# Optimization experiments

Hardware: AMD Instinct MI355X
Metric: run time of the kernel (lower is better)

Reference implementation:

```python
import jax, jax.numpy as jnp
import numpy as np

DROPOUT_RATE = 0.1  # reference runs deterministically (dropout disabled), matching eval-mode math


def setup_inputs() -> dict:
    key = jax.random.key(0)
    k1, k2, k3 = jax.random.split(key, 3)
    BH, S, D = 32, 2048, 64   # batch*heads, seq_len, d_head
    B = 2                      # true batch (mask batch dim)
    q = jax.random.normal(k1, (BH, S, D), dtype=jnp.float32)
    k = jax.random.normal(k2, (BH, S, D), dtype=jnp.float32)
    v = jax.random.normal(k3, (BH, S, D), dtype=jnp.float32)
    mask = jnp.zeros((B, S, S), dtype=jnp.float32)  # additive mask
    return {"q": q, "k": k, "v": v, "mask": mask}


def reference(q, k, v, mask):
    # Scaled dot-product attention with additive mask.
    # q,k,v: [BH, S, D]; mask: [B, S, S], tiled along batch to BH.
    dk = jnp.asarray(k.shape[-1], dtype=jnp.float32)
    scores = jnp.einsum('bqd,bkd->bqk', q, k) / jnp.sqrt(dk)  # [BH, S, S]
    reps = q.shape[0] // mask.shape[0]
    mask_t = jnp.tile(mask, (reps, 1, 1))                     # [BH, S, S]
    attn = jax.nn.softmax(scores + mask_t, axis=-1)
    out = jnp.einsum('bqk,bkd->bqd', attn, v)                 # [BH, S, D]
    # K.dropout omitted: deterministic reference (eval mode / identity)
    return out
```

## Files before the change

### kernel.cpp

```cpp
#include <hip/hip_runtime.h>


constexpr int cBH = 32;
constexpr int cS  = 2048;
constexpr int cD  = 64;
constexpr int cQT = 128;
constexpr int cNT = cS / 64;

typedef __bf16 bf16x8 __attribute__((ext_vector_type(8)));
typedef __bf16 bf16x4 __attribute__((ext_vector_type(4)));
typedef float  f32x4  __attribute__((ext_vector_type(4)));

__device__ __forceinline__ unsigned short bfbits(float f) {
    return __builtin_bit_cast(unsigned short, (__bf16)f);
}
__device__ __forceinline__ bf16x4 pack4(f32x4 a) {
    bf16x4 r;
    r[0] = (__bf16)a[0]; r[1] = (__bf16)a[1];
    r[2] = (__bf16)a[2]; r[3] = (__bf16)a[3];
    return r;
}
__device__ __forceinline__ bf16x8 pack8(f32x4 a, f32x4 b) {
    bf16x8 r;
    r[0] = (__bf16)a[0]; r[1] = (__bf16)a[1];
    r[2] = (__bf16)a[2]; r[3] = (__bf16)a[3];
    r[4] = (__bf16)b[0]; r[5] = (__bf16)b[1];
    r[6] = (__bf16)b[2]; r[7] = (__bf16)b[3];
    return r;
}
__device__ __forceinline__ int fkey(int row) {
    return ((row & 7) ^ ((row >> 3) << 1)) & 7;
}

__global__ __launch_bounds__(512, 4)
void sdpa_flash_kernel(const float* __restrict__ q,
                       const float* __restrict__ k,
                       const float* __restrict__ v,
                       const float* __restrict__ mask,
                       float* __restrict__ out)
{
    __shared__ unsigned short sK[2][64 * 64];
    __shared__ unsigned short sV[2][64 * 64];
    __shared__ unsigned short sP[8][16 * 64];

    const int tid  = threadIdx.x;
    const int wv   = tid >> 6;
    const int lane = tid & 63;
    const int quad = lane >> 4;
    const int ln   = lane & 15;

    const int fid = blockIdx.x;
    const int bh  = (fid & 7) | ((fid >> 7) << 3);
    const int qb  = ((fid >> 3) & 15) * cQT;
    const int mb  = bh & 1;

    bf16x8 aq0, aq1;
    {
        const float* qp = q + ((size_t)bh * cS + qb + wv * 16 + ln) * cD + quad * 8;
        aq0 = pack8(*(const f32x4*)(qp),      *(const f32x4*)(qp + 4));
        aq1 = pack8(*(const f32x4*)(qp + 32), *(const f32x4*)(qp + 36));
    }

    f32x4 acc[4];
    float lsum[4];
#pragma unroll
    for (int t = 0; t < 4; ++t) acc[t] = (f32x4){0.f, 0.f, 0.f, 0.f};
#pragma unroll
    for (int r = 0; r < 4; ++r) lsum[r] = 0.f;

    const float L2E = 1.4426950408889634f;
    const float SCL = 0.125f * L2E;

    const int srow = tid >> 4;
    const int col4 = (tid & 15) << 2;
    const int ka0  = srow * 64 + (((col4 >> 3) ^ (srow & 7)) << 3) + (col4 & 7);
    const int ka1  = ka0 + 32 * 64;
    const float* kg = k + (size_t)bh * cS * cD;
    const float* vg = v + (size_t)bh * cS * cD;
    const int g0 = tid * 4, g1 = 2048 + tid * 4;
    const float* mbase = mask + (size_t)mb * cS * cS
                              + (size_t)(qb + wv * 16 + quad * 4) * cS + ln;

    f32x4 K0 = *(const f32x4*)(kg + g0);
    f32x4 K1 = *(const f32x4*)(kg + g1);
    f32x4 V0 = *(const f32x4*)(vg + g0);
    f32x4 V1 = *(const f32x4*)(vg + g1);
    *(bf16x4*)&sK[0][ka0] = pack4(K0);
    *(bf16x4*)&sK[0][ka1] = pack4(K1);
#pragma unroll
    for (int j = 0; j < 4; ++j) {
        int d = col4 + j, g = (d ^ (d >> 3)) & 7;
        sV[0][d * 64 + (((srow >> 3) ^ g) << 3) + (srow & 7)]       = bfbits(V0[j]);
        sV[0][d * 64 + ((((srow >> 3) + 4) ^ g) << 3) + (srow & 7)] = bfbits(V1[j]);
    }

    for (int kt = 0; kt < cNT; ++kt) {
        const int cur = kt & 1;
        const unsigned short* sKc = sK[cur];
        const unsigned short* sVc = sV[cur];

        if (kt + 1 < cNT) {
            const int tb = (kt + 1) * 4096;
            K0 = *(const f32x4*)(kg + tb + g0);
            K1 = *(const f32x4*)(kg + tb + g1);
            V0 = *(const f32x4*)(vg + tb + g0);
            V1 = *(const f32x4*)(vg + tb + g1);
        }

        __syncthreads();

        float mrg[4][4];
#pragma unroll
        for (int nt = 0; nt < 4; ++nt)
#pragma unroll
            for (int r = 0; r < 4; ++r)
                mrg[nt][r] = mbase[(size_t)r * cS + kt * 64 + nt * 16];

        float p4[4][4];
#pragma unroll
        for (int nt = 0; nt < 4; ++nt) {
            f32x4 c = (f32x4){0.f, 0.f, 0.f, 0.f};
#pragma unroll
            for (int ks = 0; ks < 2; ++ks) {
                bf16x8 b = *(const bf16x8*)(
                    &sKc[(nt * 16 + ln) * 64 + ((((ks << 2) | quad) ^ (ln & 7)) << 3)]);
                c = __builtin_amdgcn_mfma_f32_16x16x32_bf16(ks ? aq1 : aq0, b, c, 0, 0, 0);
            }
#pragma unroll
            for (int r = 0; r < 4; ++r)
                p4[nt][r] = __builtin_amdgcn_exp2f(c[r] * SCL + mrg[nt][r] * L2E);
        }
#pragma unroll
        for (int r = 0; r < 4; ++r)
            lsum[r] += (p4[0][r] + p4[1][r]) + (p4[2][r] + p4[3][r]);

#pragma unroll
        for (int nt = 0; nt < 4; ++nt)
#pragma unroll
            for (int r = 0; r < 4; ++r) {
                int row = quad * 4 + r;
                int blk = ((nt * 2 + (ln >> 3)) ^ fkey(row)) << 3;
                sP[wv][row * 64 + blk + (ln & 7)] = bfbits(p4[nt][r]);
            }

#pragma unroll
        for (int ks = 0; ks < 2; ++ks) {
            bf16x8 ap = *(const bf16x8*)(
                &sP[wv][ln * 64 + ((((ks << 2) | quad) ^ fkey(ln)) << 3)]);
#pragma unroll
            for (int dt = 0; dt < 4; ++dt) {
                int d = dt * 16 + ln, g = (d ^ (d >> 3)) & 7;
                bf16x8 bv = *(const bf16x8*)(
                    &sVc[d * 64 + ((((ks << 2) | quad) ^ g) << 3)]);
                acc[dt] = __builtin_amdgcn_mfma_f32_16x16x32_bf16(ap, bv, acc[dt], 0, 0, 0);
            }
        }

        if (kt + 1 < cNT) {
            unsigned short* sKn = sK[cur ^ 1];
            unsigned short* sVn = sV[cur ^ 1];
            *(bf16x4*)&sKn[ka0] = pack4(K0);
            *(bf16x4*)&sKn[ka1] = pack4(K1);
#pragma unroll
            for (int j = 0; j < 4; ++j) {
                int d = col4 + j, g = (d ^ (d >> 3)) & 7;
                sVn[d * 64 + (((srow >> 3) ^ g) << 3) + (srow & 7)]       = bfbits(V0[j]);
                sVn[d * 64 + ((((srow >> 3) + 4) ^ g) << 3) + (srow & 7)] = bfbits(V1[j]);
            }
        }
    }

#pragma unroll
    for (int off = 1; off < 16; off <<= 1)
#pragma unroll
        for (int r = 0; r < 4; ++r)
            lsum[r] += __shfl_xor(lsum[r], off, 64);
    float rl[4];
#pragma unroll
    for (int r = 0; r < 4; ++r) rl[r] = 1.0f / lsum[r];
#pragma unroll
    for (int dt = 0; dt < 4; ++dt)
#pragma unroll
        for (int r = 0; r < 4; ++r)
            out[((size_t)bh * cS + qb + wv * 16 + quad * 4 + r) * cD + dt * 16 + ln]
                = acc[dt][r] * rl[r];
}

extern "C" void kernel_launch(void* const* d_in, const int* in_sizes, int n_in,
                              void* d_out, int out_size, void* d_ws, size_t ws_size,
                              hipStream_t stream) {
    const float* q = (const float*)d_in[0];
    const float* k = (const float*)d_in[1];
    const float* v = (const float*)d_in[2];
    const float* m = (const float*)d_in[3];
    float* o = (float*)d_out;
    sdpa_flash_kernel<<<dim3(512), 512, 0, stream>>>(q, k, v, m, o);
}
```

Before: 213.0 us.

## Software-pipeline PV matmul one tile behind QK, prefetch mask, prescale Q

The P·V product for tile kt-1 now runs after the QK/softmax of tile kt, using a triple-buffered V array and a double-buffered per-wave P buffer, so the two MFMA phases can interleave and the P store-to-load latency is hidden. Mask values for the next tile are prefetched into registers along with K/V instead of being loaded after the barrier. Q is prescaled by the softmax scale times log2(e) at load time, which removes a multiply per score. The cost is extra LDS (one more V buffer plus doubled P buffers) and more registers, which may hurt occupancy at the launch bound of four blocks per CU. The Q prescale also rounds slightly differently in bf16.

```diff
diff --git a/kernel.cpp b/kernel.cpp
--- a/kernel.cpp
+++ b/kernel.cpp
@@ -20,12 +20,12 @@
     r[2] = (__bf16)a[2]; r[3] = (__bf16)a[3];
     return r;
 }
-__device__ __forceinline__ bf16x8 pack8(f32x4 a, f32x4 b) {
+__device__ __forceinline__ bf16x8 pack8s(f32x4 a, f32x4 b, float s) {
     bf16x8 r;
-    r[0] = (__bf16)a[0]; r[1] = (__bf16)a[1];
-    r[2] = (__bf16)a[2]; r[3] = (__bf16)a[3];
-    r[4] = (__bf16)b[0]; r[5] = (__bf16)b[1];
-    r[6] = (__bf16)b[2]; r[7] = (__bf16)b[3];
+    r[0] = (__bf16)(a[0]*s); r[1] = (__bf16)(a[1]*s);
+    r[2] = (__bf16)(a[2]*s); r[3] = (__bf16)(a[3]*s);
+    r[4] = (__bf16)(b[0]*s); r[5] = (__bf16)(b[1]*s);
+    r[6] = (__bf16)(b[2]*s); r[7] = (__bf16)(b[3]*s);
     return r;
 }
 __device__ __forceinline__ int fkey(int row) {
@@ -40,8 +40,8 @@
                        float* __restrict__ out)
 {
     __shared__ unsigned short sK[2][64 * 64];
-    __shared__ unsigned short sV[2][64 * 64];
-    __shared__ unsigned short sP[8][16 * 64];
+    __shared__ unsigned short sV[3][64 * 64];
+    __shared__ unsigned short sP[8][2][16 * 64];
 
     const int tid  = threadIdx.x;
     const int wv   = tid >> 6;
@@ -54,11 +54,13 @@
     const int qb  = ((fid >> 3) & 15) * cQT;
     const int mb  = bh & 1;
 
+    const float L2E = 1.4426950408889634f;
+
     bf16x8 aq0, aq1;
     {
         const float* qp = q + ((size_t)bh * cS + qb + wv * 16 + ln) * cD + quad * 8;
-        aq0 = pack8(*(const f32x4*)(qp),      *(const f32x4*)(qp + 4));
-        aq1 = pack8(*(const f32x4*)(qp + 32), *(const f32x4*)(qp + 36));
+        aq0 = pack8s(*(const f32x4*)(qp),      *(const f32x4*)(qp + 4),  0.125f * L2E);
+        aq1 = pack8s(*(const f32x4*)(qp + 32), *(const f32x4*)(qp + 36), 0.125f * L2E);
     }
 
     f32x4 acc[4];
@@ -67,9 +69,6 @@
     for (int t = 0; t < 4; ++t) acc[t] = (f32x4){0.f, 0.f, 0.f, 0.f};
 #pragma unroll
     for (int r = 0; r < 4; ++r) lsum[r] = 0.f;
-
-    const float L2E = 1.4426950408889634f;
-    const float SCL = 0.125f * L2E;
 
     const int srow = tid >> 4;
     const int col4 = (tid & 15) << 2;
@@ -78,44 +77,60 @@
     const float* kg = k + (size_t)bh * cS * cD;
     const float* vg = v + (size_t)bh * cS * cD;
     const int g0 = tid * 4, g1 = 2048 + tid * 4;
-    const float* mbase = mask + (size_t)mb * cS * cS
-                              + (size_t)(qb + wv * 16 + quad * 4) * cS + ln;
-
-    f32x4 K0 = *(const f32x4*)(kg + g0);
-    f32x4 K1 = *(const f32x4*)(kg + g1);
-    f32x4 V0 = *(const f32x4*)(vg + g0);
-    f32x4 V1 = *(const f32x4*)(vg + g1);
-    *(bf16x4*)&sK[0][ka0] = pack4(K0);
-    *(bf16x4*)&sK[0][ka1] = pack4(K1);
-#pragma unroll
-    for (int j = 0; j < 4; ++j) {
-        int d = col4 + j, g = (d ^ (d >> 3)) & 7;
-        sV[0][d * 64 + (((srow >> 3) ^ g) << 3) + (srow & 7)]       = bfbits(V0[j]);
-        sV[0][d * 64 + ((((srow >> 3) + 4) ^ g) << 3) + (srow & 7)] = bfbits(V1[j]);
-    }
+
+    const float* mr0 = mask + (size_t)mb * cS * cS
+                            + (size_t)(qb + wv * 16 + quad * 4) * cS + ln;
+    const float* mr1 = mr0 + cS;
+    const float* mr2 = mr0 + 2 * cS;
+    const float* mr3 = mr0 + 3 * cS;
+
+    {
+        f32x4 K0 = *(const f32x4*)(kg + g0);
+        f32x4 K1 = *(const f32x4*)(kg + g1);
+        f32x4 V0 = *(const f32x4*)(vg + g0);
+        f32x4 V1 = *(const f32x4*)(vg + g1);
+        *(bf16x4*)&sK[0][ka0] = pack4(K0);
+        *(bf16x4*)&sK[0][ka1] = pack4(K1);
+#pragma unroll
+        for (int j = 0; j < 4; ++j) {
+            int d = col4 + j, g = (d ^ (d >> 3)) & 7;
+            sV[0][d * 64 + (((srow >> 3) ^ g) << 3) + (srow & 7)]       = bfbits(V0[j]);
+            sV[0][d * 64 + ((((srow >> 3) + 4) ^ g) << 3) + (srow & 7)] = bfbits(V1[j]);
+        }
+    }
+    float mc[16];
+#pragma unroll
+    for (int nt = 0; nt < 4; ++nt) {
+        mc[nt * 4 + 0] = mr0[nt * 16]; mc[nt * 4 + 1] = mr1[nt * 16];
+        mc[nt * 4 + 2] = mr2[nt * 16]; mc[nt * 4 + 3] = mr3[nt * 16];
+    }
+    mr0 += 64; mr1 += 64; mr2 += 64; mr3 += 64;
+
+    int vprv = 2, vcur = 0, vnxt = 1;
 
     for (int kt = 0; kt < cNT; ++kt) {
-        const int cur = kt & 1;
-        const unsigned short* sKc = sK[cur];
-        const unsigned short* sVc = sV[cur];
-
+        const int kcur = kt & 1;
+
+        f32x4 K0, K1, V0, V1;
+        float mn[16];
         if (kt + 1 < cNT) {
             const int tb = (kt + 1) * 4096;
             K0 = *(const f32x4*)(kg + tb + g0);
             K1 = *(const f32x4*)(kg + tb + g1);
             V0 = *(const f32x4*)(vg + tb + g0);
             V1 = *(const f32x4*)(vg + tb + g1);
+#pragma unroll
+            for (int nt = 0; nt < 4; ++nt) {
+                mn[nt * 4 + 0] = mr0[nt * 16]; mn[nt * 4 + 1] = mr1[nt * 16];
+                mn[nt * 4 + 2] = mr2[nt * 16]; mn[nt * 4 + 3] = mr3[nt * 16];
+            }
+            mr0 += 64; mr1 += 64; mr2 += 64; mr3 += 64;
         }
 
         __syncthreads();
 
-        float mrg[4][4];
-#pragma unroll
-        for (int nt = 0; nt < 4; ++nt)
-#pragma unroll
-            for (int r = 0; r < 4; ++r)
-                mrg[nt][r] = mbase[(size_t)r * cS + kt * 64 + nt * 16];
-
+        const unsigned short* sKc = sK[kcur];
+        unsigned short* sPw = &sP[wv][kcur][0];
         float p4[4][4];
 #pragma unroll
         for (int nt = 0; nt < 4; ++nt) {
@@ -128,37 +143,40 @@
             }
 #pragma unroll
             for (int r = 0; r < 4; ++r)
-                p4[nt][r] = __builtin_amdgcn_exp2f(c[r] * SCL + mrg[nt][r] * L2E);
+                p4[nt][r] = __builtin_amdgcn_exp2f(fmaf(mc[nt * 4 + r], L2E, c[r]));
         }
 #pragma unroll
         for (int r = 0; r < 4; ++r)
             lsum[r] += (p4[0][r] + p4[1][r]) + (p4[2][r] + p4[3][r]);
-
 #pragma unroll
         for (int nt = 0; nt < 4; ++nt)
 #pragma unroll
             for (int r = 0; r < 4; ++r) {
                 int row = quad * 4 + r;
                 int blk = ((nt * 2 + (ln >> 3)) ^ fkey(row)) << 3;
-                sP[wv][row * 64 + blk + (ln & 7)] = bfbits(p4[nt][r]);
-            }
-
-#pragma unroll
-        for (int ks = 0; ks < 2; ++ks) {
-            bf16x8 ap = *(const bf16x8*)(
-                &sP[wv][ln * 64 + ((((ks << 2) | quad) ^ fkey(ln)) << 3)]);
-#pragma unroll
-            for (int dt = 0; dt < 4; ++dt) {
-                int d = dt * 16 + ln, g = (d ^ (d >> 3)) & 7;
-                bf16x8 bv = *(const bf16x8*)(
-                    &sVc[d * 64 + ((((ks << 2) | quad) ^ g) << 3)]);
-                acc[dt] = __builtin_amdgcn_mfma_f32_16x16x32_bf16(ap, bv, acc[dt], 0, 0, 0);
+                sPw[row * 64 + blk + (ln & 7)] = bfbits(p4[nt][r]);
+            }
+
+        if (kt > 0) {
+            const unsigned short* sPr = &sP[wv][kcur ^ 1][0];
+            const unsigned short* sVp = sV[vprv];
+#pragma unroll
+            for (int ks = 0; ks < 2; ++ks) {
+                bf16x8 ap = *(const bf16x8*)(
+                    &sPr[ln * 64 + ((((ks << 2) | quad) ^ fkey(ln)) << 3)]);
+#pragma unroll
+                for (int dt = 0; dt < 4; ++dt) {
+                    int d = dt * 16 + ln, g = (d ^ (d >> 3)) & 7;
+                    bf16x8 bv = *(const bf16x8*)(
+                        &sVp[d * 64 + ((((ks << 2) | quad) ^ g) << 3)]);
+                    acc[dt] = __builtin_amdgcn_mfma_f32_16x16x32_bf16(ap, bv, acc[dt], 0, 0, 0);
+                }
             }
         }
 
         if (kt + 1 < cNT) {
-            unsigned short* sKn = sK[cur ^ 1];
-            unsigned short* sVn = sV[cur ^ 1];
+            unsigned short* sKn = sK[kcur ^ 1];
+            unsigned short* sVn = sV[vnxt];
             *(bf16x4*)&sKn[ka0] = pack4(K0);
             *(bf16x4*)&sKn[ka1] = pack4(K1);
 #pragma unroll
@@ -166,6 +184,27 @@
                 int d = col4 + j, g = (d ^ (d >> 3)) & 7;
                 sVn[d * 64 + (((srow >> 3) ^ g) << 3) + (srow & 7)]       = bfbits(V0[j]);
                 sVn[d * 64 + ((((srow >> 3) + 4) ^ g) << 3) + (srow & 7)] = bfbits(V1[j]);
+            }
+#pragma unroll
+            for (int i = 0; i < 16; ++i) mc[i] = mn[i];
+        }
+
+        int t = vprv; vprv = vcur; vcur = vnxt; vnxt = t;
+    }
+
+    {
+        const unsigned short* sPr = &sP[wv][(cNT - 1) & 1][0];
+        const unsigned short* sVp = sV[vprv];
+#pragma unroll
+        for (int ks = 0; ks < 2; ++ks) {
+            bf16x8 ap = *(const bf16x8*)(
+                &sPr[ln * 64 + ((((ks << 2) | quad) ^ fkey(ln)) << 3)]);
+#pragma unroll
+            for (int dt = 0; dt < 4; ++dt) {
+                int d = dt * 16 + ln, g = (d ^ (d >> 3)) & 7;
+                bf16x8 bv = *(const bf16x8*)(
+                    &sVp[d * 64 + ((((ks << 2) | quad) ^ g) << 3)]);
+                acc[dt] = __builtin_amdgcn_mfma_f32_16x16x32_bf16(ap, bv, acc[dt], 0, 0, 0);
             }
         }
     }
```

Result: slower. 301.3 us (+41.5%).
